# Kernel optimization log

Measured on AMD Instinct MI355X. Metric: run time of the kernel, lower is better.

The kernel has to match this reference:

```python
import jax, jax.numpy as jnp
import numpy as np

B, S, D = 2, 2048, 2048
NH, NKV = 16, 4
HD = D // NH          # 128
Q_DIM = NH * HD       # 2048
KV_DIM = NKV * HD     # 512
N_REP = NH // NKV     # 4


def setup_inputs() -> dict:
    key = jax.random.key(0)
    k1, k2, k3, k4 = jax.random.split(key, 4)
    x = jax.random.normal(k1, (B, S, D), dtype=jnp.float32)
    freqs_cis = jax.random.normal(k2, (S, HD), dtype=jnp.float32)
    Wqkv = jax.random.normal(k3, (Q_DIM + 2 * KV_DIM, D), dtype=jnp.float32) * (D ** -0.5)
    Wo = jax.random.normal(k4, (D, Q_DIM), dtype=jnp.float32) * (Q_DIM ** -0.5)
    return {"x": x, "freqs_cis": freqs_cis, "Wqkv": Wqkv, "Wo": Wo}


def _apply_rope(xq, xk, freqs_cis):
    # xq: [B,S,NH,HD], xk: [B,S,NKV,HD], freqs_cis: [S,HD] viewed as [S,1,HD//2,2]
    f = freqs_cis.reshape(S, 1, HD // 2, 2)
    f0, f1 = f[..., 0], f[..., 1]  # broadcast over batch & heads

    def rot(t):
        shp = t.shape
        tp = t.reshape(*shp[:-1], HD // 2, 2)
        t0, t1 = tp[..., 0], tp[..., 1]
        # row1 = <x, (f0,f1)>;  row0 = <x, (f1,-f0)>  (matches torch flip+negate)
        row1 = t0 * f0 + t1 * f1
        row0 = t0 * f1 - t1 * f0
        return jnp.stack([row0, row1], axis=-1).reshape(shp)

    return rot(xq), rot(xk)


def reference(x, freqs_cis, Wqkv, Wo):
    # Fused QKV projection (exact path: all RLA sketch dims = 0)
    xqkv = jnp.einsum('bsd,od->bso', x, Wqkv)
    xq = xqkv[..., :Q_DIM].reshape(B, S, NH, HD)
    xk = xqkv[..., Q_DIM:Q_DIM + KV_DIM].reshape(B, S, NKV, HD)
    xv = xqkv[..., Q_DIM + KV_DIM:].reshape(B, S, NKV, HD)

    xq, xk = _apply_rope(xq, xk, freqs_cis)

    # [B,H,S,HD]
    xq = xq.transpose(0, 2, 1, 3)
    xk = xk.transpose(0, 2, 1, 3)
    xv = xv.transpose(0, 2, 1, 3)

    # GQA: repeat kv heads n_rep times
    xk = jnp.repeat(xk, N_REP, axis=1)
    xv = jnp.repeat(xv, N_REP, axis=1)

    scale = 1.0 / jnp.sqrt(jnp.asarray(HD, dtype=xq.dtype))
    scores = jnp.einsum('bhqd,bhkd->bhqk', xq, xk) * scale
    causal = jnp.tril(jnp.ones((S, S), dtype=bool))
    scores = jnp.where(causal, scores, jnp.finfo(scores.dtype).min)
    probs = jax.nn.softmax(scores, axis=-1)
    out = jnp.einsum('bhqk,bhkd->bhqd', probs, xv)  # [B,H,S,HD]

    out = out.transpose(0, 2, 1, 3).reshape(B, S, Q_DIM)
    return jnp.einsum('bsq,dq->bsd', out, Wo)
```

## Files before the change

kernel.cpp:

```cpp
#include <hip/hip_runtime.h>
#include <hip/hip_bf16.h>
#include <cstdint>
#include <cstddef>

#define B_ 2
#define S_ 2048
#define NH_ 16
#define NKV_ 4
#define HD_ 128
#define QDIM_ 2048
#define KVDIM_ 512
#define QKV_ 3072

typedef __attribute__((ext_vector_type(8))) short short8;
typedef __attribute__((ext_vector_type(4))) short bhalf4;
typedef __attribute__((ext_vector_type(4))) float float4v;

__device__ __forceinline__ float bf2f(short u) {
  union { unsigned int i; float f; } v;
  v.i = ((unsigned int)(unsigned short)u) << 16;
  return v.f;
}
__device__ __forceinline__ short f2bf(float f) {
  union { float f; unsigned int i; } v; v.f = f;
  unsigned int x = v.i;
  x += 0x7fffu + ((x >> 16) & 1u);
  return (short)(x >> 16);
}

#if __has_builtin(__builtin_amdgcn_exp2f)
__device__ __forceinline__ float exp2fast(float x) { return __builtin_amdgcn_exp2f(x); }
#else
__device__ __forceinline__ float exp2fast(float x) { return exp2f(x); }
#endif

__device__ __forceinline__ unsigned int cvt_pk_bf16(float a, float b) {
  unsigned int r;
  asm("v_cvt_pk_bf16_f32 %0, %1, %2" : "=v"(r) : "v"(a), "v"(b));
  return r;
}

__device__ __forceinline__ void async_copy16(void* lds, const void* g) {
  __builtin_amdgcn_global_load_lds(
      (const __attribute__((address_space(1))) void*)g,
      (__attribute__((address_space(3))) void*)lds, 16, 0, 0);
}

__device__ __forceinline__ void cvt8(const float* f, short* d) {
  float4v a = *(const float4v*)(f);
  float4v b = *(const float4v*)(f + 4);
  short8 r;
#pragma unroll
  for (int e = 0; e < 4; ++e) { r[e] = f2bf(a[e]); r[4 + e] = f2bf(b[e]); }
  *(short8*)d = r;
}

__global__ void f32_to_bf16(const float* __restrict__ src, short* __restrict__ dst,
                            int n8) {
  int id = blockIdx.x * 256 + threadIdx.x;
  if (id >= n8) return;
  cvt8(src + (size_t)id * 8, dst + (size_t)id * 8);
}

__global__ void f32_to_bf16_2(const float* __restrict__ s0, short* __restrict__ d0,
                              int n0_8, const float* __restrict__ s1,
                              short* __restrict__ d1) {
  int id = blockIdx.x * 256 + threadIdx.x;
  if (id < n0_8) {
    cvt8(s0 + (size_t)id * 8, d0 + (size_t)id * 8);
  } else {
    int j = id - n0_8;
    cvt8(s1 + (size_t)j * 8, d1 + (size_t)j * 8);
  }
}

template <int N, int K, bool CF32>
__global__ __launch_bounds__(256)
void gemm_nt_bf16(const short* __restrict__ A, const short* __restrict__ Bm,
                  void* __restrict__ Cp) {
  __shared__ __align__(16) short sA[128 * 32];
  __shared__ __align__(16) short sB[128 * 32];
  const int tid = threadIdx.x;
  const int m0 = blockIdx.y * 128, n0 = blockIdx.x * 128;
  const int wave = tid >> 6, lane = tid & 63;
  const int wm = (wave & 1) << 6, wn = (wave >> 1) << 6;
  const int lm = lane & 15, kg = lane >> 4;

  float4v acc[4][4];
#pragma unroll
  for (int i = 0; i < 4; ++i)
#pragma unroll
    for (int j = 0; j < 4; ++j)
      acc[i][j] = (float4v){0.f, 0.f, 0.f, 0.f};

  const int r0 = tid >> 2, c0 = tid & 3;
  const short* gA0 = A + (size_t)(m0 + r0) * K + c0 * 8;
  const short* gA1 = gA0 + (size_t)64 * K;
  const short* gB0 = Bm + (size_t)(n0 + r0) * K + c0 * 8;
  const short* gB1 = gB0 + (size_t)64 * K;
  short* lA0 = sA + tid * 8;
  short* lA1 = sA + 2048 + tid * 8;
  short* lB0 = sB + tid * 8;
  short* lB1 = sB + 2048 + tid * 8;

  for (int k0 = 0; k0 < K; k0 += 32) {
    async_copy16(lA0, gA0 + k0);
    async_copy16(lA1, gA1 + k0);
    async_copy16(lB0, gB0 + k0);
    async_copy16(lB1, gB1 + k0);
    __syncthreads();

    short8 a[4], b[4];
#pragma unroll
    for (int i = 0; i < 4; ++i)
      a[i] = *(const short8*)(sA + (wm + i * 16 + lm) * 32 + kg * 8);
#pragma unroll
    for (int j = 0; j < 4; ++j)
      b[j] = *(const short8*)(sB + (wn + j * 16 + lm) * 32 + kg * 8);
#pragma unroll
    for (int i = 0; i < 4; ++i)
#pragma unroll
      for (int j = 0; j < 4; ++j)
        acc[i][j] = __builtin_amdgcn_mfma_f32_16x16x32_bf16(a[i], b[j], acc[i][j], 0, 0, 0);
    __syncthreads();
  }

#pragma unroll
  for (int i = 0; i < 4; ++i) {
    const int rb = m0 + wm + i * 16 + kg * 4;
#pragma unroll
    for (int j = 0; j < 4; ++j) {
      const int cc = n0 + wn + j * 16 + lm;
#pragma unroll
      for (int r = 0; r < 4; ++r) {
        if constexpr (CF32)
          ((float*)Cp)[(size_t)(rb + r) * N + cc] = acc[i][j][r];
        else
          ((short*)Cp)[(size_t)(rb + r) * N + cc] = f2bf(acc[i][j][r]);
      }
    }
  }
}

__global__ void rope_split(const short* __restrict__ xqkv, const float* __restrict__ freqs,
                           short* __restrict__ Qr, short* __restrict__ Kr,
                           short* __restrict__ Vv) {
  const int id = blockIdx.x * 256 + threadIdx.x;
  const int i = id / (QKV_ / 8);
  const int c8 = id % (QKV_ / 8);
  const int col = c8 * 8;
  const int b = i >> 11, s = i & (S_ - 1);
  short8 xv = *(const short8*)(xqkv + (size_t)i * QKV_ + col);
  if (col < QDIM_ + KVDIM_) {
    int d;
    short* dst;
    float sc;
    if (col < QDIM_) {
      int hh = col >> 7; d = col & 127;
      dst = Qr + ((size_t)(b * NH_ + hh) * S_ + s) * HD_ + d;
      sc = 0.12751744543795287f;
    } else {
      int cc = col - QDIM_;
      int hh = cc >> 7; d = cc & 127;
      dst = Kr + ((size_t)(b * NKV_ + hh) * S_ + s) * HD_ + d;
      sc = 1.0f;
    }
    const float* fp = freqs + (size_t)s * HD_ + d;
    float4v fa = *(const float4v*)(fp);
    float4v fb = *(const float4v*)(fp + 4);
    float ff[8] = {fa[0], fa[1], fa[2], fa[3], fb[0], fb[1], fb[2], fb[3]};
    short8 ov;
#pragma unroll
    for (int pp = 0; pp < 4; ++pp) {
      float t0 = bf2f(xv[2 * pp]), t1 = bf2f(xv[2 * pp + 1]);
      float f0 = ff[2 * pp], f1 = ff[2 * pp + 1];
      ov[2 * pp]     = f2bf((t0 * f1 - t1 * f0) * sc);
      ov[2 * pp + 1] = f2bf((t0 * f0 + t1 * f1) * sc);
    }
    *(short8*)dst = ov;
  } else {
    int cc = col - QDIM_ - KVDIM_;
    int hh = cc >> 7, d = cc & 127;
    *(short8*)(Vv + ((size_t)(b * NKV_ + hh) * S_ + s) * HD_ + d) = xv;
  }
}

__global__ void transpose_v(const short* __restrict__ Vv, short* __restrict__ Vt) {
  __shared__ short t[64][72];
  const int s0 = blockIdx.x * 64, d0 = blockIdx.y * 64;
  const short* src = Vv + (size_t)blockIdx.z * S_ * HD_;
  short* dst = Vt + (size_t)blockIdx.z * S_ * HD_;
  const int tid = threadIdx.x;
#pragma unroll
  for (int c = 0; c < 2; ++c) {
    int ch = tid + 256 * c;
    int row = ch >> 3, kc = ch & 7;
    *(short8*)(&t[row][kc * 8]) =
        *(const short8*)(src + (size_t)(s0 + row) * HD_ + d0 + kc * 8);
  }
  __syncthreads();
#pragma unroll
  for (int c = 0; c < 2; ++c) {
    int ch = tid + 256 * c;
    int drow = ch >> 3, sc = ch & 7;
    short8 w;
#pragma unroll
    for (int j = 0; j < 8; ++j) w[j] = t[sc * 8 + j][drow];
    *(short8*)(dst + (size_t)(d0 + drow) * S_ + s0 + sc * 8) = w;
  }
}

#define TK 64

__global__ __launch_bounds__(256, 2)
void attn_causal(const short* __restrict__ Q, const short* __restrict__ K,
                 const short* __restrict__ Vt, short* __restrict__ O) {
  const int bh = blockIdx.x;
  const int by = blockIdx.y;
  const int qt = (by < 8) ? (15 - by) : (by - 8);
  const int b = bh >> 4, h = bh & 15;
  const int kvh = h >> 2;
  const int tid = threadIdx.x, wave = tid >> 6, lane = tid & 63;
  const int lm = lane & 15, kg = lane >> 4;

  __shared__ __align__(16) short sK[TK * HD_];
  __shared__ __align__(16) short sVt[HD_ * TK];

  const short* Qb = Q + (size_t)(b * NH_ + h) * S_ * HD_;
  const short* Kb = K + (size_t)(b * NKV_ + kvh) * S_ * HD_;
  const short* Vtb = Vt + (size_t)(b * NKV_ + kvh) * S_ * HD_;

  auto stageK = [&](int k0) {
#pragma unroll
    for (int c = 0; c < 4; ++c) {
      int ch = tid + 256 * c;
      int row = ch >> 4, kc = ch & 15;
      async_copy16(sK + ch * 8,
                   Kb + (size_t)(k0 + row) * HD_ + (kc ^ (row & 7)) * 8);
    }
  };
  auto stageV = [&](int k0) {
#pragma unroll
    for (int c = 0; c < 4; ++c) {
      int ch = tid + 256 * c;
      int row = ch >> 3, kc = ch & 7;
      async_copy16(sVt + ch * 8,
                   Vtb + (size_t)row * S_ + k0 + (kc ^ (row & 7)) * 8);
    }
  };

  const int qbase = qt * 128 + wave * 32 + lm;
  short8 qf[2][4];
#pragma unroll
  for (int u = 0; u < 2; ++u)
#pragma unroll
    for (int kk = 0; kk < 4; ++kk)
      qf[u][kk] = *(const short8*)(Qb + (size_t)(qbase + u * 16) * HD_ +
                                   kk * 32 + kg * 8);

  float mcur[2] = {-1e9f, -1e9f}, lcur[2] = {0.f, 0.f};
  float4v o[2][8];
#pragma unroll
  for (int u = 0; u < 2; ++u)
#pragma unroll
    for (int df = 0; df < 8; ++df) o[u][df] = (float4v){0.f, 0.f, 0.f, 0.f};

  stageK(0);
  const int nst = 2 * qt + 2;
  for (int s = 0; s < nst; ++s) {
    const int k0 = s * TK;
    const bool last = (s == nst - 1);
    const bool maskstep = (s >= nst - 2);

    __syncthreads();
    stageV(k0);

    float4v sf[2][4];
#pragma unroll
    for (int u = 0; u < 2; ++u)
#pragma unroll
      for (int mj = 0; mj < 4; ++mj) sf[u][mj] = (float4v){0.f, 0.f, 0.f, 0.f};
    __builtin_amdgcn_s_setprio(1);
#pragma unroll
    for (int kk = 0; kk < 4; ++kk) {
      int kd = kk * 4 + kg;
#pragma unroll
      for (int mj = 0; mj < 4; ++mj) {
        int row = mj * 16 + lm;
        short8 af = *(const short8*)(sK + row * HD_ + (kd ^ (row & 7)) * 8);
        sf[0][mj] = __builtin_amdgcn_mfma_f32_16x16x32_bf16(af, qf[0][kk], sf[0][mj], 0, 0, 0);
        sf[1][mj] = __builtin_amdgcn_mfma_f32_16x16x32_bf16(af, qf[1][kk], sf[1][mj], 0, 0, 0);
      }
    }
    __builtin_amdgcn_s_setprio(0);

    if (maskstep) {
#pragma unroll
      for (int u = 0; u < 2; ++u) {
        const int qg = qbase + u * 16;
#pragma unroll
        for (int mj = 0; mj < 4; ++mj)
#pragma unroll
          for (int r = 0; r < 4; ++r) {
            int kcol = k0 + mj * 16 + kg * 4 + r;
            sf[u][mj][r] = (kcol <= qg) ? sf[u][mj][r] : -3e38f;
          }
      }
    }

    bhalf4 pb[2][4];
    bool need[2];
    float alpha[2];
#pragma unroll
    for (int u = 0; u < 2; ++u) {
      float mx = -3e38f;
#pragma unroll
      for (int mj = 0; mj < 4; ++mj)
#pragma unroll
        for (int r = 0; r < 4; ++r) mx = fmaxf(mx, sf[u][mj][r]);
      mx = fmaxf(mx, __shfl_xor(mx, 16, 64));
      mx = fmaxf(mx, __shfl_xor(mx, 32, 64));
      need[u] = (mx > mcur[u] + 4.f);
      const float mnew = fmaxf(mcur[u], mx);
      alpha[u] = need[u] ? exp2fast(mcur[u] - mnew) : 1.f;
      const float m_use = need[u] ? mnew : mcur[u];
      float rs = 0.f;
#pragma unroll
      for (int t = 0; t < 4; ++t) {
        float e0 = exp2fast(sf[u][t][0] - m_use);
        float e1 = exp2fast(sf[u][t][1] - m_use);
        float e2 = exp2fast(sf[u][t][2] - m_use);
        float e3 = exp2fast(sf[u][t][3] - m_use);
        rs += (e0 + e1) + (e2 + e3);
        union { unsigned int w[2]; bhalf4 v; } pk;
        pk.w[0] = cvt_pk_bf16(e0, e1);
        pk.w[1] = cvt_pk_bf16(e2, e3);
        pb[u][t] = pk.v;
      }
      rs += __shfl_xor(rs, 16, 64);
      rs += __shfl_xor(rs, 32, 64);
      mcur[u] = m_use;
      lcur[u] = lcur[u] * alpha[u] + rs;
    }

    __syncthreads();
    if (!last) stageK(k0 + TK);

#pragma unroll
    for (int u = 0; u < 2; ++u) {
      if (__any(need[u])) {
#pragma unroll
        for (int df = 0; df < 8; ++df)
#pragma unroll
          for (int r = 0; r < 4; ++r) o[u][df][r] *= alpha[u];
      }
    }

    __builtin_amdgcn_s_setprio(1);
#pragma unroll
    for (int t = 0; t < 4; ++t) {
      int kc = t * 2 + (kg >> 1);
#pragma unroll
      for (int df = 0; df < 8; ++df) {
        int row = df * 16 + lm;
        bhalf4 va = *(const bhalf4*)(sVt + row * TK + (kc ^ (row & 7)) * 8 +
                                     (kg & 1) * 4);
        o[0][df] = __builtin_amdgcn_mfma_f32_16x16x16bf16_1k(va, pb[0][t], o[0][df], 0, 0, 0);
        o[1][df] = __builtin_amdgcn_mfma_f32_16x16x16bf16_1k(va, pb[1][t], o[1][df], 0, 0, 0);
      }
    }
    __builtin_amdgcn_s_setprio(0);
  }

#pragma unroll
  for (int u = 0; u < 2; ++u) {
    const float inv = 1.f / lcur[u];
    const size_t rowoff =
        (size_t)(b * S_ + qbase + u * 16) * QDIM_ + h * HD_ + kg * 4;
#pragma unroll
    for (int df = 0; df < 8; ++df) {
      bhalf4 w;
      w[0] = f2bf(o[u][df][0] * inv);
      w[1] = f2bf(o[u][df][1] * inv);
      w[2] = f2bf(o[u][df][2] * inv);
      w[3] = f2bf(o[u][df][3] * inv);
      *(bhalf4*)(O + rowoff + df * 16) = w;
    }
  }
}

extern "C" void kernel_launch(void* const* d_in, const int* in_sizes, int n_in,
                              void* d_out, int out_size, void* d_ws, size_t ws_size,
                              hipStream_t stream) {
  const float* x     = (const float*)d_in[0];
  const float* freqs = (const float*)d_in[1];
  const float* Wqkv  = (const float*)d_in[2];
  const float* Wo    = (const float*)d_in[3];
  float* out = (float*)d_out;

  short* ws     = (short*)d_ws;
  short* xb     = ws;
  short* Wob    = ws;
  short* Wqkvb  = ws + (size_t)4096 * 2048;
  short* xqkv   = Wqkvb + (size_t)QKV_ * 2048;
  short* attn   = xqkv;
  short* Qr     = xqkv + (size_t)4096 * QKV_;
  short* Kr     = Qr + (size_t)B_ * NH_ * S_ * HD_;
  short* Vv     = Kr + (size_t)B_ * NKV_ * S_ * HD_;
  short* Vtg    = Vv + (size_t)B_ * NKV_ * S_ * HD_;

  f32_to_bf16_2<<<(4096 * 2048 / 8 + QKV_ * 2048 / 8) / 256, 256, 0, stream>>>(
      x, xb, 4096 * 2048 / 8, Wqkv, Wqkvb);
  gemm_nt_bf16<QKV_, 2048, false>
      <<<dim3(QKV_ / 128, 4096 / 128), 256, 0, stream>>>(xb, Wqkvb, xqkv);
  f32_to_bf16<<<(2048 * 2048 / 8) / 256, 256, 0, stream>>>(Wo, Wob, 2048 * 2048 / 8);
  rope_split<<<(B_ * S_ * QKV_ / 8) / 256, 256, 0, stream>>>(xqkv, freqs, Qr, Kr, Vv);
  transpose_v<<<dim3(S_ / 64, HD_ / 64, B_ * NKV_), 256, 0, stream>>>(Vv, Vtg);
  attn_causal<<<dim3(32, 16), 256, 0, stream>>>(Qr, Kr, Vtg, attn);
  gemm_nt_bf16<2048, 2048, true>
      <<<dim3(2048 / 128, 4096 / 128), 256, 0, stream>>>(attn, Wob, out);
}
```

Measured before the change: 326.9 us.

## Add 256x256-tile double-buffered GEMM with swizzled LDS for QKV projection

Adds a new GEMM kernel with 256x256 output tiles and 512 threads. It double-buffers K=64 stages split into two halves, uses async global-to-LDS copies, an XOR-swizzled LDS layout to avoid bank conflicts, and raised wave priority around the MFMA bursts. The kernel is used only for the QKV projection. The goal is more data reuse per tile and overlap of loads with compute. In exchange the grid shrinks to 12x16=192 blocks, which may leave some CUs idle, and register pressure rises with 32 accumulators per wave.

```diff
diff --git a/kernel.cpp b/kernel.cpp
--- a/kernel.cpp
+++ b/kernel.cpp
@@ -127,6 +127,127 @@
 
 #pragma unroll
   for (int i = 0; i < 4; ++i) {
+    const int rb = m0 + wm + i * 16 + kg * 4;
+#pragma unroll
+    for (int j = 0; j < 4; ++j) {
+      const int cc = n0 + wn + j * 16 + lm;
+#pragma unroll
+      for (int r = 0; r < 4; ++r) {
+        if constexpr (CF32)
+          ((float*)Cp)[(size_t)(rb + r) * N + cc] = acc[i][j][r];
+        else
+          ((short*)Cp)[(size_t)(rb + r) * N + cc] = f2bf(acc[i][j][r]);
+      }
+    }
+  }
+}
+
+template <int N, int K, bool CF32>
+__global__ __launch_bounds__(512, 1)
+void gemm_nt_256(const short* __restrict__ A, const short* __restrict__ Bm,
+                 void* __restrict__ Cp) {
+  __shared__ __align__(16) short sA[2][2][256 * 32];
+  __shared__ __align__(16) short sB[2][2][256 * 32];
+  const int tid = threadIdx.x;
+  const int wid = tid >> 6, lane = tid & 63;
+  const int lm = lane & 15, kg = lane >> 4;
+  const int wm = (wid >> 2) * 128, wn = (wid & 3) * 64;
+  const int m0 = blockIdx.y * 256, n0 = blockIdx.x * 256;
+
+  const short* A0 = A + (size_t)m0 * K;
+  const short* B0 = Bm + (size_t)n0 * K;
+
+  auto stage = [&](const short* src0, short* dstHalf, int t, int kh) {
+#pragma unroll
+    for (int q = 0; q < 2; ++q) {
+      const int ch = tid + 512 * q;
+      const int r = ch >> 2, c = ch & 3;
+      async_copy16(dstHalf + ch * 8,
+                   src0 + (size_t)r * K + t * 64 + kh * 32 +
+                       (c ^ ((r >> 1) & 3)) * 8);
+    }
+  };
+  auto ldA = [&](int bf, int kh, int i) {
+    const int R = wm + i * 16 + lm;
+    return *(const short8*)(&sA[bf][kh][R * 32 + (kg ^ ((R >> 1) & 3)) * 8]);
+  };
+  auto ldB = [&](int bf, int kh, int j) {
+    const int R = wn + j * 16 + lm;
+    return *(const short8*)(&sB[bf][kh][R * 32 + (kg ^ ((R >> 1) & 3)) * 8]);
+  };
+
+  float4v acc[8][4];
+#pragma unroll
+  for (int i = 0; i < 8; ++i)
+#pragma unroll
+    for (int j = 0; j < 4; ++j)
+      acc[i][j] = (float4v){0.f, 0.f, 0.f, 0.f};
+
+  stage(A0, &sA[0][0][0], 0, 0);
+  stage(B0, &sB[0][0][0], 0, 0);
+  stage(A0, &sA[0][1][0], 0, 1);
+  stage(B0, &sB[0][1][0], 0, 1);
+  asm volatile("s_waitcnt vmcnt(4)" ::: "memory");
+  asm volatile("s_barrier" ::: "memory");
+  __builtin_amdgcn_sched_barrier(0);
+
+  const int NT = K / 64;
+  for (int t = 0; t < NT; ++t) {
+    const int bf = t & 1, nbf = bf ^ 1;
+    const bool haveNext = (t + 1 < NT);
+
+    {
+      short8 ar[8], br[4];
+#pragma unroll
+      for (int i = 0; i < 8; ++i) ar[i] = ldA(bf, 0, i);
+#pragma unroll
+      for (int j = 0; j < 4; ++j) br[j] = ldB(bf, 0, j);
+      if (haveNext) {
+        stage(A0, &sA[nbf][0][0], t + 1, 0);
+        stage(B0, &sB[nbf][0][0], t + 1, 0);
+      }
+      asm volatile("s_barrier" ::: "memory");
+      __builtin_amdgcn_s_setprio(1);
+#pragma unroll
+      for (int i = 0; i < 8; ++i)
+#pragma unroll
+        for (int j = 0; j < 4; ++j)
+          acc[i][j] = __builtin_amdgcn_mfma_f32_16x16x32_bf16(ar[i], br[j], acc[i][j], 0, 0, 0);
+      __builtin_amdgcn_s_setprio(0);
+      if (haveNext) asm volatile("s_waitcnt vmcnt(4)" ::: "memory");
+      else          asm volatile("s_waitcnt vmcnt(0)" ::: "memory");
+      asm volatile("s_barrier" ::: "memory");
+      __builtin_amdgcn_sched_barrier(0);
+    }
+
+    {
+      short8 ar[8], br[4];
+#pragma unroll
+      for (int i = 0; i < 8; ++i) ar[i] = ldA(bf, 1, i);
+#pragma unroll
+      for (int j = 0; j < 4; ++j) br[j] = ldB(bf, 1, j);
+      if (haveNext) {
+        stage(A0, &sA[nbf][1][0], t + 1, 1);
+        stage(B0, &sB[nbf][1][0], t + 1, 1);
+      }
+      asm volatile("s_barrier" ::: "memory");
+      __builtin_amdgcn_s_setprio(1);
+#pragma unroll
+      for (int i = 0; i < 8; ++i)
+#pragma unroll
+        for (int j = 0; j < 4; ++j)
+          acc[i][j] = __builtin_amdgcn_mfma_f32_16x16x32_bf16(ar[i], br[j], acc[i][j], 0, 0, 0);
+      __builtin_amdgcn_s_setprio(0);
+      if (haveNext) {
+        asm volatile("s_waitcnt vmcnt(4)" ::: "memory");
+        asm volatile("s_barrier" ::: "memory");
+        __builtin_amdgcn_sched_barrier(0);
+      }
+    }
+  }
+
+#pragma unroll
+  for (int i = 0; i < 8; ++i) {
     const int rb = m0 + wm + i * 16 + kg * 4;
 #pragma unroll
     for (int j = 0; j < 4; ++j) {
@@ -411,8 +532,8 @@
 
   f32_to_bf16_2<<<(4096 * 2048 / 8 + QKV_ * 2048 / 8) / 256, 256, 0, stream>>>(
       x, xb, 4096 * 2048 / 8, Wqkv, Wqkvb);
-  gemm_nt_bf16<QKV_, 2048, false>
-      <<<dim3(QKV_ / 128, 4096 / 128), 256, 0, stream>>>(xb, Wqkvb, xqkv);
+  gemm_nt_256<QKV_, 2048, false>
+      <<<dim3(QKV_ / 256, 4096 / 256), 512, 0, stream>>>(xb, Wqkvb, xqkv);
   f32_to_bf16<<<(2048 * 2048 / 8) / 256, 256, 0, stream>>>(Wo, Wob, 2048 * 2048 / 8);
   rope_split<<<(B_ * S_ * QKV_ / 8) / 256, 256, 0, stream>>>(xqkv, freqs, Qr, Kr, Vv);
   transpose_v<<<dim3(S_ / 64, HD_ / 64, B_ * NKV_), 256, 0, stream>>>(Vv, Vtg);
```

Result: faster. 319.6 us (-2.2%).
